# Kernel tuning notes

Hardware: AMD Instinct MI355X
Metric: run time of the kernel (lower is better)

## Reference

```python
import jax, jax.numpy as jnp
import numpy as np

TOP_K = 16
NUM_HEADS = 1
EPS = 1e-8  # torch F.cosine_similarity eps


def setup_inputs() -> dict:
    key = jax.random.key(0)
    ks = jax.random.split(key, 8)
    B, N, Dk, Dv = 64, 8192, 256, 256
    return {
        "query": jax.random.normal(ks[0], (B, Dk), jnp.float32),
        "key_memory": jax.random.normal(ks[1], (B, N, Dk), jnp.float32),
        "value_memory": jax.random.normal(ks[2], (B, N, Dv), jnp.float32),
        "iteration": jax.random.randint(ks[3], (B, 1), 0, N),
        "in_proj_w": jax.random.normal(ks[4], (3 * Dv, Dv), jnp.float32) * 0.06,
        "in_proj_b": jnp.zeros((3 * Dv,), jnp.float32),
        "out_proj_w": jax.random.normal(ks[5], (Dv, Dv), jnp.float32) * 0.06,
        "out_proj_b": jnp.zeros((Dv,), jnp.float32),
    }


def _mha(x, in_w, in_b, out_w, out_b):
    # torch nn.MultiheadAttention (batch_first, qkv same embed dim) self-attention
    B, T, E = x.shape
    H = NUM_HEADS
    hd = E // H
    qkv = x @ in_w.T + in_b                      # [B,T,3E]
    q, k, v = jnp.split(qkv, 3, axis=-1)

    def heads(t):
        return t.reshape(B, T, H, hd).transpose(0, 2, 1, 3)  # [B,H,T,hd]

    q, k, v = heads(q), heads(k), heads(v)
    scale = jnp.asarray(1.0 / np.sqrt(hd), x.dtype)
    attn = jax.nn.softmax(jnp.einsum('bhqd,bhkd->bhqk', q, k) * scale, axis=-1)
    o = jnp.einsum('bhqk,bhkd->bhqd', attn, v).transpose(0, 2, 1, 3).reshape(B, T, E)
    return o @ out_w.T + out_b


def reference(query, key_memory, value_memory, iteration,
              in_proj_w, in_proj_b, out_proj_w, out_proj_b):
    B, N, Dv = value_memory.shape
    # memory validity mask: item n is valid iff n <= iteration[b]
    mem_idx = jnp.arange(N)[None, :]                                   # [1,N]
    mask = (mem_idx <= iteration).astype(key_memory.dtype)[..., None]  # [B,N,1]
    km = key_memory * mask
    vm = value_memory * mask

    # masked cosine similarity between each memory key and the query
    num = jnp.einsum('bnd,bd->bn', km, query)                          # [B,N]
    denom = jnp.maximum(
        jnp.linalg.norm(km, axis=-1) * jnp.linalg.norm(query, axis=-1, keepdims=True),
        EPS)
    sim = num / denom                                                  # [B,N]

    topk_sim, topk_idx = jax.lax.top_k(sim, TOP_K)                     # [B,K]
    topk_vm = jnp.take_along_axis(vm, topk_idx[:, :, None], axis=1)    # [B,K,Dv]

    wv = jax.nn.softmax(topk_sim, axis=-1)[..., None]                  # [B,K,1]
    nrv = wv * topk_vm                                                 # [B,K,Dv]

    nrv = _mha(nrv, in_proj_w, in_proj_b, out_proj_w, out_proj_b)      # [B,K,Dv]

    # rows with iteration == 0 are left as zeros (scatter of computed rows)
    not_first = (iteration.reshape(-1) > 0).astype(nrv.dtype)[:, None, None]
    nrv = nrv * not_first
    return nrv.sum(axis=1)                                             # [B,Dv]
```

## Files before the change

### kernel.cpp

```cpp
#include <hip/hip_runtime.h>
#include <hip/hip_bf16.h>
#include <math.h>

#define B_  64
#define N_  8192
#define D_  256
#define K_  16
#define NCHUNK_ 32
#define EPS_ 1e-8f
#define NEG_ -3.4e38f

static const size_t CANDV_OFF = 0;
static const size_t CANDI_OFF = 32768;
static const size_t XT_OFF    = 65536;
static const size_t WT_OFF    = 65536 + 262144;
static const size_t WOT_OFF   = WT_OFF + 196608;
static const size_t QKV_OFF   = WOT_OFF + 65536;

__global__ void __launch_bounds__(256)
prep_kernel(const float* __restrict__ inw, const float* __restrict__ ow,
            float* __restrict__ WT, float* __restrict__ WoT) {
    int idx = blockIdx.x * blockDim.x + threadIdx.x;
    if (idx < 768 * 256) {
        int d = idx / 768, r = idx - d * 768;
        WT[idx] = inw[r * 256 + d];
    } else {
        int idx2 = idx - 768 * 256;
        if (idx2 < 256 * 256) {
            int d = idx2 >> 8, r = idx2 & 255;
            WoT[idx2] = ow[r * 256 + d];
        }
    }
}

__global__ void __launch_bounds__(256)
simtopk_kernel(const float* __restrict__ q, const float* __restrict__ km,
               const int* __restrict__ iter,
               float* __restrict__ cand_v, int* __restrict__ cand_i) {
    int b = blockIdx.x >> 5;
    int chunk = blockIdx.x & (NCHUNK_ - 1);
    int tid = threadIdx.x;
    int w = tid >> 6;
    int lane = tid & 63;
    int it = iter[b];

    __shared__ float svals[256];
    __shared__ float rv4[4];
    __shared__ int   ri4[4];

    float4 qv = ((const float4*)(q + (size_t)b * D_))[lane];
    float qq = qv.x*qv.x + qv.y*qv.y + qv.z*qv.z + qv.w*qv.w;
    for (int off = 32; off; off >>= 1) qq += __shfl_xor(qq, off);
    float qn = sqrtf(qq);

    for (int j = 0; j < 64; j++) {
        int l = (j << 2) + w;
        int n = chunk + (l << 5);
        float s = 0.f;
        if (n <= it) {
            float4 kv = ((const float4*)(km + ((size_t)b * N_ + n) * D_))[lane];
            float dot = kv.x*qv.x + kv.y*qv.y + kv.z*qv.z + kv.w*qv.w;
            float sq  = kv.x*kv.x + kv.y*kv.y + kv.z*kv.z + kv.w*kv.w;
            for (int off = 32; off; off >>= 1) {
                dot += __shfl_xor(dot, off);
                sq  += __shfl_xor(sq,  off);
            }
            s = dot / fmaxf(sqrtf(sq) * qn, EPS_);
        }
        if (lane == 0) svals[l] = s;
    }
    __syncthreads();

    float v = svals[tid];
    int   idx = chunk + (tid << 5);
    for (int sel = 0; sel < K_; sel++) {
        float bv = v; int bi = idx;
        for (int off = 32; off; off >>= 1) {
            float ov = __shfl_xor(bv, off);
            int   oi = __shfl_xor(bi, off);
            if (ov > bv || (ov == bv && oi < bi)) { bv = ov; bi = oi; }
        }
        if (lane == 0) { rv4[w] = bv; ri4[w] = bi; }
        __syncthreads();
        float wv0 = rv4[0]; int wi0 = ri4[0];
        #pragma unroll
        for (int w2 = 1; w2 < 4; w2++) {
            float ov = rv4[w2]; int oi = ri4[w2];
            if (ov > wv0 || (ov == wv0 && oi < wi0)) { wv0 = ov; wi0 = oi; }
        }
        if (idx == wi0) v = NEG_;
        if (tid == 0) {
            cand_v[(size_t)blockIdx.x * K_ + sel] = wv0;
            cand_i[(size_t)blockIdx.x * K_ + sel] = wi0;
        }
        __syncthreads();
    }
}

__global__ void __launch_bounds__(256)
merge_gather_kernel(const float* __restrict__ cand_v, const int* __restrict__ cand_i,
                    const float* __restrict__ vm, const int* __restrict__ iter,
                    float* __restrict__ xT) {
    int b = blockIdx.x, tid = threadIdx.x;
    int w = tid >> 6, lane = tid & 63;
    int it = iter[b];
    float v0 = cand_v[(size_t)b * 512 + tid];
    float v1 = cand_v[(size_t)b * 512 + 256 + tid];
    int   i0 = cand_i[(size_t)b * 512 + tid];
    int   i1 = cand_i[(size_t)b * 512 + 256 + tid];
    __shared__ float selv[K_];
    __shared__ int   seli[K_];
    __shared__ float w16[K_];
    __shared__ float rv4[4];
    __shared__ int   ri4[4];
    for (int sel = 0; sel < K_; sel++) {
        float bv; int bi;
        if (v1 > v0 || (v1 == v0 && i1 < i0)) { bv = v1; bi = i1; }
        else                                  { bv = v0; bi = i0; }
        for (int off = 32; off; off >>= 1) {
            float ov = __shfl_xor(bv, off);
            int   oi = __shfl_xor(bi, off);
            if (ov > bv || (ov == bv && oi < bi)) { bv = ov; bi = oi; }
        }
        if (lane == 0) { rv4[w] = bv; ri4[w] = bi; }
        __syncthreads();
        float wv0 = rv4[0]; int wi0 = ri4[0];
        #pragma unroll
        for (int w2 = 1; w2 < 4; w2++) {
            float ov = rv4[w2]; int oi = ri4[w2];
            if (ov > wv0 || (ov == wv0 && oi < wi0)) { wv0 = ov; wi0 = oi; }
        }
        if (i0 == wi0) v0 = NEG_;
        if (i1 == wi0) v1 = NEG_;
        if (tid == 0) { selv[sel] = wv0; seli[sel] = wi0; }
        __syncthreads();
    }
    if (tid < K_) {
        float m = NEG_;
        for (int jj = 0; jj < K_; jj++) m = fmaxf(m, selv[jj]);
        float ssum = 0.f;
        for (int jj = 0; jj < K_; jj++) ssum += expf(selv[jj] - m);
        w16[tid] = expf(selv[tid] - m) / ssum;
    }
    __syncthreads();
    float* xb = xT + (size_t)b * (D_ * K_);
    #pragma unroll
    for (int k = 0; k < K_; k++) {
        int row = seli[k];
        float val = 0.f;
        if (row <= it) val = w16[k] * vm[((size_t)b * N_ + row) * D_ + tid];
        xb[tid * K_ + k] = val;
    }
}

__global__ void __launch_bounds__(256)
qkv_kernel(const float* __restrict__ xT, const float* __restrict__ WT,
           const float* __restrict__ inb, float* __restrict__ qkv) {
    int b = blockIdx.x / 3, which = blockIdx.x % 3;
    int tid = threadIdx.x;
    float acc[K_];
    #pragma unroll
    for (int k = 0; k < K_; k++) acc[k] = 0.f;
    const float* xb = xT + (size_t)b * (D_ * K_);
    const float* wt = WT + which * 256 + tid;
    #pragma unroll 4
    for (int d = 0; d < D_; d++) {
        float wgt = wt[(size_t)d * 768];
        float4 x0 = ((const float4*)(xb + d * K_))[0];
        float4 x1 = ((const float4*)(xb + d * K_))[1];
        float4 x2 = ((const float4*)(xb + d * K_))[2];
        float4 x3 = ((const float4*)(xb + d * K_))[3];
        acc[0]  += x0.x * wgt; acc[1]  += x0.y * wgt; acc[2]  += x0.z * wgt; acc[3]  += x0.w * wgt;
        acc[4]  += x1.x * wgt; acc[5]  += x1.y * wgt; acc[6]  += x1.z * wgt; acc[7]  += x1.w * wgt;
        acc[8]  += x2.x * wgt; acc[9]  += x2.y * wgt; acc[10] += x2.z * wgt; acc[11] += x2.w * wgt;
        acc[12] += x3.x * wgt; acc[13] += x3.y * wgt; acc[14] += x3.z * wgt; acc[15] += x3.w * wgt;
    }
    float bias = inb[which * 256 + tid];
    #pragma unroll
    for (int k = 0; k < K_; k++)
        qkv[(((size_t)b * 3 + which) * K_ + k) * D_ + tid] = acc[k] + bias;
}

__global__ void __launch_bounds__(256)
final_kernel(const float* __restrict__ qkv, const int* __restrict__ iter,
             const float* __restrict__ WoT, const float* __restrict__ ob,
             float* __restrict__ out) {
    int b = blockIdx.x, tid = threadIdx.x;
    int it = iter[b];
    if (it == 0) { out[(size_t)b * D_ + tid] = 0.f; return; }
    __shared__ float qs[K_][D_ + 1];
    __shared__ float ks[K_][D_ + 1];
    __shared__ float vs[K_][D_ + 1];
    __shared__ float attn[K_][K_];
    __shared__ float colsum[K_];
    __shared__ float so[D_];
    const float* base = qkv + (size_t)b * 3 * K_ * D_;
    #pragma unroll
    for (int k = 0; k < K_; k++) {
        qs[k][tid] = base[(0 * K_ + k) * D_ + tid];
        ks[k][tid] = base[(1 * K_ + k) * D_ + tid];
        vs[k][tid] = base[(2 * K_ + k) * D_ + tid];
    }
    __syncthreads();
    int i = tid >> 4, j = tid & 15;
    float s = 0.f;
    for (int d = 0; d < D_; d++) s += qs[i][d] * ks[j][d];
    attn[i][j] = s * 0.0625f;
    __syncthreads();
    if (tid < K_) {
        float m = NEG_;
        for (int jj = 0; jj < K_; jj++) m = fmaxf(m, attn[tid][jj]);
        float ssum = 0.f;
        for (int jj = 0; jj < K_; jj++) ssum += expf(attn[tid][jj] - m);
        float inv = 1.f / ssum;
        for (int jj = 0; jj < K_; jj++) attn[tid][jj] = expf(attn[tid][jj] - m) * inv;
    }
    __syncthreads();
    if (tid < K_) {
        float c = 0.f;
        for (int ii = 0; ii < K_; ii++) c += attn[ii][tid];
        colsum[tid] = c;
    }
    __syncthreads();
    float acc = 0.f;
    #pragma unroll
    for (int jj = 0; jj < K_; jj++) acc += colsum[jj] * vs[jj][tid];
    so[tid] = acc;
    __syncthreads();
    float o = 0.f;
    for (int e = 0; e < D_; e++) o += so[e] * WoT[e * D_ + tid];
    out[(size_t)b * D_ + tid] = o + 16.f * ob[tid];
}

extern "C" void kernel_launch(void* const* d_in, const int* in_sizes, int n_in,
                              void* d_out, int out_size, void* d_ws, size_t ws_size,
                              hipStream_t stream) {
    const float* q   = (const float*)d_in[0];
    const float* km  = (const float*)d_in[1];
    const float* vm  = (const float*)d_in[2];
    const int*   it  = (const int*)  d_in[3];
    const float* inw = (const float*)d_in[4];
    const float* inb = (const float*)d_in[5];
    const float* ow  = (const float*)d_in[6];
    const float* ob  = (const float*)d_in[7];
    float* out = (float*)d_out;

    float* ws     = (float*)d_ws;
    float* cand_v = ws + CANDV_OFF;
    int*   cand_i = (int*)(ws + CANDI_OFF);
    float* xT     = ws + XT_OFF;
    float* WT     = ws + WT_OFF;
    float* WoT    = ws + WOT_OFF;
    float* qkv    = ws + QKV_OFF;

    prep_kernel<<<dim3(1024), dim3(256), 0, stream>>>(inw, ow, WT, WoT);
    simtopk_kernel<<<dim3(B_ * NCHUNK_), dim3(256), 0, stream>>>(q, km, it, cand_v, cand_i);
    merge_gather_kernel<<<dim3(B_), dim3(256), 0, stream>>>(cand_v, cand_i, vm, it, xT);
    qkv_kernel<<<dim3(B_ * 3), dim3(256), 0, stream>>>(xT, WT, inb, qkv);
    final_kernel<<<dim3(B_), dim3(256), 0, stream>>>(qkv, it, WoT, ob, out);
}
```

Before: 160.1 us.

## Skip invalid key chunks, per-wave top-k, fuse merge with QKV projection

The similarity kernel now assigns contiguous 64-row slices to each wave and exits early when the slice lies beyond the iteration limit, so masked memory rows are never read. Each wave produces its own top-16 without block-level barriers. The merge step selects from 2048 candidates and computes the QKV projection from shared memory in the same kernel. The weight-transpose prep kernel is removed in favour of row-wise float4 reads of the original weights. The cost is that the merge is repeated three times per batch and the merge itself grows larger. Skipped slices write zero-valued placeholder candidates, which relies on valid similarities ranking correctly against them.

After: 128.6 us. -19.7%, faster.

```diff
diff --git a/kernel.cpp b/kernel.cpp
--- a/kernel.cpp
+++ b/kernel.cpp
@@ -2,121 +2,118 @@
 #include <hip/hip_bf16.h>
 #include <math.h>
 
-#define B_  64
-#define N_  8192
-#define D_  256
-#define K_  16
-#define NCHUNK_ 32
+#define B_   64
+#define N_   8192
+#define D_   256
+#define K_   16
+#define NCH_ 32
+#define CPB_ 2048
 #define EPS_ 1e-8f
 #define NEG_ -3.4e38f
 
 static const size_t CANDV_OFF = 0;
-static const size_t CANDI_OFF = 32768;
-static const size_t XT_OFF    = 65536;
-static const size_t WT_OFF    = 65536 + 262144;
-static const size_t WOT_OFF   = WT_OFF + 196608;
-static const size_t QKV_OFF   = WOT_OFF + 65536;
-
-__global__ void __launch_bounds__(256)
-prep_kernel(const float* __restrict__ inw, const float* __restrict__ ow,
-            float* __restrict__ WT, float* __restrict__ WoT) {
-    int idx = blockIdx.x * blockDim.x + threadIdx.x;
-    if (idx < 768 * 256) {
-        int d = idx / 768, r = idx - d * 768;
-        WT[idx] = inw[r * 256 + d];
-    } else {
-        int idx2 = idx - 768 * 256;
-        if (idx2 < 256 * 256) {
-            int d = idx2 >> 8, r = idx2 & 255;
-            WoT[idx2] = ow[r * 256 + d];
-        }
-    }
-}
+static const size_t CANDI_OFF = 131072;
+static const size_t QKV_OFF   = 262144;
 
 __global__ void __launch_bounds__(256)
 simtopk_kernel(const float* __restrict__ q, const float* __restrict__ km,
                const int* __restrict__ iter,
                float* __restrict__ cand_v, int* __restrict__ cand_i) {
-    int b = blockIdx.x >> 5;
-    int chunk = blockIdx.x & (NCHUNK_ - 1);
-    int tid = threadIdx.x;
-    int w = tid >> 6;
-    int lane = tid & 63;
-    int it = iter[b];
+    int b     = blockIdx.x >> 5;
+    int chunk = blockIdx.x & (NCH_ - 1);
+    int tid   = threadIdx.x;
+    int w     = tid >> 6;
+    int lane  = tid & 63;
+    int g     = lane >> 4;
+    int p     = lane & 15;
+    int it    = iter[b];
+    int r0    = (chunk << 8) + (w << 6);
+    size_t cbase = ((size_t)blockIdx.x * 4 + w) * K_;
+
+    if (r0 > it) {
+        if (lane < K_) { cand_v[cbase + lane] = 0.f; cand_i[cbase + lane] = r0 + lane; }
+        return;
+    }
 
     __shared__ float svals[256];
-    __shared__ float rv4[4];
-    __shared__ int   ri4[4];
-
-    float4 qv = ((const float4*)(q + (size_t)b * D_))[lane];
-    float qq = qv.x*qv.x + qv.y*qv.y + qv.z*qv.z + qv.w*qv.w;
-    for (int off = 32; off; off >>= 1) qq += __shfl_xor(qq, off);
+
+    float4 q4[4];
+    #pragma unroll
+    for (int k = 0; k < 4; k++)
+        q4[k] = *(const float4*)(q + (size_t)b * D_ + k * 64 + p * 4);
+    float qq = 0.f;
+    #pragma unroll
+    for (int k = 0; k < 4; k++)
+        qq += q4[k].x*q4[k].x + q4[k].y*q4[k].y + q4[k].z*q4[k].z + q4[k].w*q4[k].w;
+    #pragma unroll
+    for (int off = 8; off; off >>= 1) qq += __shfl_xor(qq, off);
     float qn = sqrtf(qq);
 
-    for (int j = 0; j < 64; j++) {
-        int l = (j << 2) + w;
-        int n = chunk + (l << 5);
+    for (int t = 0; t < 16; t++) {
+        int r = r0 + (t << 2) + g;
         float s = 0.f;
-        if (n <= it) {
-            float4 kv = ((const float4*)(km + ((size_t)b * N_ + n) * D_))[lane];
-            float dot = kv.x*qv.x + kv.y*qv.y + kv.z*qv.z + kv.w*qv.w;
-            float sq  = kv.x*kv.x + kv.y*kv.y + kv.z*kv.z + kv.w*kv.w;
-            for (int off = 32; off; off >>= 1) {
+        if (r <= it) {
+            const float* rp = km + ((size_t)b * N_ + r) * D_;
+            float dot = 0.f, sq = 0.f;
+            #pragma unroll
+            for (int k = 0; k < 4; k++) {
+                float4 kv = *(const float4*)(rp + k * 64 + p * 4);
+                dot += kv.x*q4[k].x + kv.y*q4[k].y + kv.z*q4[k].z + kv.w*q4[k].w;
+                sq  += kv.x*kv.x + kv.y*kv.y + kv.z*kv.z + kv.w*kv.w;
+            }
+            #pragma unroll
+            for (int off = 8; off; off >>= 1) {
                 dot += __shfl_xor(dot, off);
                 sq  += __shfl_xor(sq,  off);
             }
             s = dot / fmaxf(sqrtf(sq) * qn, EPS_);
         }
-        if (lane == 0) svals[l] = s;
-    }
-    __syncthreads();
-
-    float v = svals[tid];
-    int   idx = chunk + (tid << 5);
+        if (p == 0) svals[(w << 6) + (t << 2) + g] = s;
+    }
+
+    float v  = svals[(w << 6) + lane];
+    int  idx = r0 + lane;
     for (int sel = 0; sel < K_; sel++) {
         float bv = v; int bi = idx;
+        #pragma unroll
         for (int off = 32; off; off >>= 1) {
             float ov = __shfl_xor(bv, off);
             int   oi = __shfl_xor(bi, off);
             if (ov > bv || (ov == bv && oi < bi)) { bv = ov; bi = oi; }
         }
-        if (lane == 0) { rv4[w] = bv; ri4[w] = bi; }
-        __syncthreads();
-        float wv0 = rv4[0]; int wi0 = ri4[0];
-        #pragma unroll
-        for (int w2 = 1; w2 < 4; w2++) {
-            float ov = rv4[w2]; int oi = ri4[w2];
-            if (ov > wv0 || (ov == wv0 && oi < wi0)) { wv0 = ov; wi0 = oi; }
-        }
-        if (idx == wi0) v = NEG_;
-        if (tid == 0) {
-            cand_v[(size_t)blockIdx.x * K_ + sel] = wv0;
-            cand_i[(size_t)blockIdx.x * K_ + sel] = wi0;
-        }
-        __syncthreads();
+        if (idx == bi) v = NEG_;
+        if (lane == 0) { cand_v[cbase + sel] = bv; cand_i[cbase + sel] = bi; }
     }
 }
 
 __global__ void __launch_bounds__(256)
-merge_gather_kernel(const float* __restrict__ cand_v, const int* __restrict__ cand_i,
-                    const float* __restrict__ vm, const int* __restrict__ iter,
-                    float* __restrict__ xT) {
-    int b = blockIdx.x, tid = threadIdx.x;
-    int w = tid >> 6, lane = tid & 63;
+merge_qkv_kernel(const float* __restrict__ cand_v, const int* __restrict__ cand_i,
+                 const float* __restrict__ vm, const int* __restrict__ iter,
+                 const float* __restrict__ inw, const float* __restrict__ inb,
+                 float* __restrict__ qkv) {
+    int b = blockIdx.x / 3, which = blockIdx.x - b * 3;
+    int tid = threadIdx.x, w = tid >> 6, lane = tid & 63;
     int it = iter[b];
-    float v0 = cand_v[(size_t)b * 512 + tid];
-    float v1 = cand_v[(size_t)b * 512 + 256 + tid];
-    int   i0 = cand_i[(size_t)b * 512 + tid];
-    int   i1 = cand_i[(size_t)b * 512 + 256 + tid];
-    __shared__ float selv[K_];
-    __shared__ int   seli[K_];
+    if (it == 0) return;
+
+    float cv[8]; int ci[8];
+    #pragma unroll
+    for (int j = 0; j < 8; j++) {
+        cv[j] = cand_v[(size_t)b * CPB_ + (j << 8) + tid];
+        ci[j] = cand_i[(size_t)b * CPB_ + (j << 8) + tid];
+    }
+
+    __shared__ float rv4[4]; __shared__ int ri4[4];
+    __shared__ float selv[K_]; __shared__ int seli[K_];
     __shared__ float w16[K_];
-    __shared__ float rv4[4];
-    __shared__ int   ri4[4];
+    __shared__ float xs[D_][K_];
+
     for (int sel = 0; sel < K_; sel++) {
-        float bv; int bi;
-        if (v1 > v0 || (v1 == v0 && i1 < i0)) { bv = v1; bi = i1; }
-        else                                  { bv = v0; bi = i0; }
+        float bv = cv[0]; int bi = ci[0];
+        #pragma unroll
+        for (int j = 1; j < 8; j++)
+            if (cv[j] > bv || (cv[j] == bv && ci[j] < bi)) { bv = cv[j]; bi = ci[j]; }
+        #pragma unroll
         for (int off = 32; off; off >>= 1) {
             float ov = __shfl_xor(bv, off);
             int   oi = __shfl_xor(bi, off);
@@ -124,17 +121,16 @@
         }
         if (lane == 0) { rv4[w] = bv; ri4[w] = bi; }
         __syncthreads();
-        float wv0 = rv4[0]; int wi0 = ri4[0];
-        #pragma unroll
-        for (int w2 = 1; w2 < 4; w2++) {
-            float ov = rv4[w2]; int oi = ri4[w2];
-            if (ov > wv0 || (ov == wv0 && oi < wi0)) { wv0 = ov; wi0 = oi; }
-        }
-        if (i0 == wi0) v0 = NEG_;
-        if (i1 == wi0) v1 = NEG_;
-        if (tid == 0) { selv[sel] = wv0; seli[sel] = wi0; }
+        float wv = rv4[0]; int wi = ri4[0];
+        #pragma unroll
+        for (int w2 = 1; w2 < 4; w2++)
+            if (rv4[w2] > wv || (rv4[w2] == wv && ri4[w2] < wi)) { wv = rv4[w2]; wi = ri4[w2]; }
+        #pragma unroll
+        for (int j = 0; j < 8; j++) if (ci[j] == wi) cv[j] = NEG_;
+        if (tid == 0) { selv[sel] = wv; seli[sel] = wi; }
         __syncthreads();
     }
+
     if (tid < K_) {
         float m = NEG_;
         for (int jj = 0; jj < K_; jj++) m = fmaxf(m, selv[jj]);
@@ -143,39 +139,36 @@
         w16[tid] = expf(selv[tid] - m) / ssum;
     }
     __syncthreads();
-    float* xb = xT + (size_t)b * (D_ * K_);
+
     #pragma unroll
     for (int k = 0; k < K_; k++) {
         int row = seli[k];
-        float val = 0.f;
-        if (row <= it) val = w16[k] * vm[((size_t)b * N_ + row) * D_ + tid];
-        xb[tid * K_ + k] = val;
-    }
-}
-
-__global__ void __launch_bounds__(256)
-qkv_kernel(const float* __restrict__ xT, const float* __restrict__ WT,
-           const float* __restrict__ inb, float* __restrict__ qkv) {
-    int b = blockIdx.x / 3, which = blockIdx.x % 3;
-    int tid = threadIdx.x;
+        float val = (row <= it) ? w16[k] * vm[((size_t)b * N_ + row) * D_ + tid] : 0.f;
+        xs[tid][k] = val;
+    }
+    __syncthreads();
+
     float acc[K_];
     #pragma unroll
     for (int k = 0; k < K_; k++) acc[k] = 0.f;
-    const float* xb = xT + (size_t)b * (D_ * K_);
-    const float* wt = WT + which * 256 + tid;
-    #pragma unroll 4
-    for (int d = 0; d < D_; d++) {
-        float wgt = wt[(size_t)d * 768];
-        float4 x0 = ((const float4*)(xb + d * K_))[0];
-        float4 x1 = ((const float4*)(xb + d * K_))[1];
-        float4 x2 = ((const float4*)(xb + d * K_))[2];
-        float4 x3 = ((const float4*)(xb + d * K_))[3];
-        acc[0]  += x0.x * wgt; acc[1]  += x0.y * wgt; acc[2]  += x0.z * wgt; acc[3]  += x0.w * wgt;
-        acc[4]  += x1.x * wgt; acc[5]  += x1.y * wgt; acc[6]  += x1.z * wgt; acc[7]  += x1.w * wgt;
-        acc[8]  += x2.x * wgt; acc[9]  += x2.y * wgt; acc[10] += x2.z * wgt; acc[11] += x2.w * wgt;
-        acc[12] += x3.x * wgt; acc[13] += x3.y * wgt; acc[14] += x3.z * wgt; acc[15] += x3.w * wgt;
-    }
-    float bias = inb[which * 256 + tid];
+    const float* wrow = inw + ((size_t)(which * D_ + tid)) * D_;
+    for (int d = 0; d < D_; d += 4) {
+        float4 wv4 = *(const float4*)(wrow + d);
+        float wk[4] = {wv4.x, wv4.y, wv4.z, wv4.w};
+        #pragma unroll
+        for (int dd = 0; dd < 4; dd++) {
+            float wgt = wk[dd];
+            float4 x0 = *(const float4*)(&xs[d + dd][0]);
+            float4 x1 = *(const float4*)(&xs[d + dd][4]);
+            float4 x2 = *(const float4*)(&xs[d + dd][8]);
+            float4 x3 = *(const float4*)(&xs[d + dd][12]);
+            acc[0]  += x0.x * wgt; acc[1]  += x0.y * wgt; acc[2]  += x0.z * wgt; acc[3]  += x0.w * wgt;
+            acc[4]  += x1.x * wgt; acc[5]  += x1.y * wgt; acc[6]  += x1.z * wgt; acc[7]  += x1.w * wgt;
+            acc[8]  += x2.x * wgt; acc[9]  += x2.y * wgt; acc[10] += x2.z * wgt; acc[11] += x2.w * wgt;
+            acc[12] += x3.x * wgt; acc[13] += x3.y * wgt; acc[14] += x3.z * wgt; acc[15] += x3.w * wgt;
+        }
+    }
+    float bias = inb[which * D_ + tid];
     #pragma unroll
     for (int k = 0; k < K_; k++)
         qkv[(((size_t)b * 3 + which) * K_ + k) * D_ + tid] = acc[k] + bias;
@@ -183,7 +176,7 @@
 
 __global__ void __launch_bounds__(256)
 final_kernel(const float* __restrict__ qkv, const int* __restrict__ iter,
-             const float* __restrict__ WoT, const float* __restrict__ ob,
+             const float* __restrict__ ow, const float* __restrict__ ob,
              float* __restrict__ out) {
     int b = blockIdx.x, tid = threadIdx.x;
     int it = iter[b];
@@ -228,7 +221,12 @@
     so[tid] = acc;
     __syncthreads();
     float o = 0.f;
-    for (int e = 0; e < D_; e++) o += so[e] * WoT[e * D_ + tid];
+    const float* orow = ow + (size_t)tid * D_;
+    for (int e = 0; e < D_; e += 4) {
+        float4 wv = *(const float4*)(orow + e);
+        float4 sv = *(const float4*)(&so[e]);
+        o += sv.x * wv.x + sv.y * wv.y + sv.z * wv.z + sv.w * wv.w;
+    }
     out[(size_t)b * D_ + tid] = o + 16.f * ob[tid];
 }
 
@@ -248,14 +246,9 @@
     float* ws     = (float*)d_ws;
     float* cand_v = ws + CANDV_OFF;
     int*   cand_i = (int*)(ws + CANDI_OFF);
-    float* xT     = ws + XT_OFF;
-    float* WT     = ws + WT_OFF;
-    float* WoT    = ws + WOT_OFF;
     float* qkv    = ws + QKV_OFF;
 
-    prep_kernel<<<dim3(1024), dim3(256), 0, stream>>>(inw, ow, WT, WoT);
-    simtopk_kernel<<<dim3(B_ * NCHUNK_), dim3(256), 0, stream>>>(q, km, it, cand_v, cand_i);
-    merge_gather_kernel<<<dim3(B_), dim3(256), 0, stream>>>(cand_v, cand_i, vm, it, xT);
-    qkv_kernel<<<dim3(B_ * 3), dim3(256), 0, stream>>>(xT, WT, inb, qkv);
-    final_kernel<<<dim3(B_), dim3(256), 0, stream>>>(qkv, it, WoT, ob, out);
-}
+    simtopk_kernel<<<dim3(B_ * NCH_), dim3(256), 0, stream>>>(q, km, it, cand_v, cand_i);
+    merge_qkv_kernel<<<dim3(B_ * 3), dim3(256), 0, stream>>>(cand_v, cand_i, vm, it, inw, inb, qkv);
+    final_kernel<<<dim3(B_), dim3(256), 0, stream>>>(qkv, it, ow, ob, out);
+}
```
